# Optimization experiments

Hardware: AMD Instinct MI355X
Metric: run time of the kernel (lower is better)

Reference implementation:

```python
import jax, jax.numpy as jnp
import numpy as np

B, L, V, H, NL = 128, 512, 2048, 512, 2


def setup_inputs() -> dict:
    key = jax.random.key(0)
    ks = jax.random.split(key, 20)
    s = 0.05  # param scale
    inp = {
        "input_ids": jax.random.randint(ks[0], (B,), 0, V),
        "last_hidden": jax.random.normal(ks[1], (NL, B, H), jnp.float32),
        "word_dict_vec": jax.random.normal(ks[2], (B, V, H), jnp.float32),
        "encoder_outputs": jax.random.normal(ks[3], (L, B, H), jnp.float32),
        "seq_mask": (jax.random.uniform(ks[4], (B, L)) < 0.2).at[:, 0].set(False),
        # Attn params (torch Linear: y = x @ W.T + b)
        "attn_W": jax.random.normal(ks[5], (H, 2 * H), jnp.float32) * s,
        "attn_b": jax.random.normal(ks[6], (H,), jnp.float32) * s,
        "score_W": jax.random.normal(ks[7], (1, H), jnp.float32) * s,
        # concat layer
        "concat_W": jax.random.normal(ks[8], (H, 2 * H), jnp.float32) * s,
        "concat_b": jax.random.normal(ks[9], (H,), jnp.float32) * s,
        # GRU layer 0 (input 2H) and layer 1 (input H); gates ordered r,z,n as in torch
        "W_ih0": jax.random.normal(ks[10], (3 * H, 2 * H), jnp.float32) * s,
        "W_hh0": jax.random.normal(ks[11], (3 * H, H), jnp.float32) * s,
        "b_ih0": jax.random.normal(ks[12], (3 * H,), jnp.float32) * s,
        "b_hh0": jax.random.normal(ks[13], (3 * H,), jnp.float32) * s,
        "W_ih1": jax.random.normal(ks[14], (3 * H, H), jnp.float32) * s,
        "W_hh1": jax.random.normal(ks[15], (3 * H, H), jnp.float32) * s,
        "b_ih1": jax.random.normal(ks[16], (3 * H,), jnp.float32) * s,
        "b_hh1": jax.random.normal(ks[17], (3 * H,), jnp.float32) * s,
    }
    return inp


def _gru_cell(x, h, W_ih, W_hh, b_ih, b_hh):
    gi = x @ W_ih.T + b_ih
    gh = h @ W_hh.T + b_hh
    i_r, i_z, i_n = jnp.split(gi, 3, axis=-1)
    h_r, h_z, h_n = jnp.split(gh, 3, axis=-1)
    r = jax.nn.sigmoid(i_r + h_r)
    z = jax.nn.sigmoid(i_z + h_z)
    n = jnp.tanh(i_n + r * h_n)
    return (1.0 - z) * n + z * h


def reference(input_ids, last_hidden, word_dict_vec, encoder_outputs, seq_mask,
              attn_W, attn_b, score_W, concat_W, concat_b,
              W_ih0, W_hh0, b_ih0, b_hh0, W_ih1, W_hh1, b_ih1, b_hh1):
    # one_hot @ word_dict_vec == per-batch row gather (same math)
    emb = word_dict_vec[jnp.arange(B), input_ids]  # [B, H]

    # Bahdanau additive attention over encoder_outputs [L, B, H]
    q = last_hidden[-1]  # [B, H]
    hid = jnp.broadcast_to(q[None], (L, B, H))
    energy_in = jnp.concatenate([hid, encoder_outputs], axis=2)  # [L, B, 2H]
    e = jnp.tanh(energy_in @ attn_W.T + attn_b) @ score_W.T      # [L, B, 1]
    scores = e[..., 0].T                                          # [B, L]
    scores = jnp.where(seq_mask, jnp.float32(-1e12), scores)
    aw = jax.nn.softmax(scores, axis=1)                           # [B, L]

    context = jnp.einsum('bl,lbh->bh', aw, encoder_outputs)       # [B, H]

    # single-step 2-layer GRU (eval mode: dropout = identity)
    x0 = jnp.concatenate([emb, context], axis=1)                  # [B, 2H]
    h0 = _gru_cell(x0, last_hidden[0], W_ih0, W_hh0, b_ih0, b_hh0)
    h1 = _gru_cell(h0, last_hidden[1], W_ih1, W_hh1, b_ih1, b_hh1)
    hidden = jnp.stack([h0, h1])                                  # [2, B, H]

    output = jnp.tanh(jnp.concatenate([h1, context], axis=1) @ concat_W.T + concat_b)
    return output, hidden
```

## Files before the change

### kernel.cpp

```cpp
#include <hip/hip_runtime.h>
#include <stdint.h>

#define Hdim 512
#define Bdim 128
#define Ldim 512
#define Vdim 2048

typedef unsigned short u16;
using f32x4  = float  __attribute__((ext_vector_type(4)));
using bf16x8 = __bf16 __attribute__((ext_vector_type(8)));

__device__ inline u16 f2bf(float x) {
  uint32_t u = __float_as_uint(x);
  u += 0x7fffu + ((u >> 16) & 1u);
  return (u16)(u >> 16);
}
__device__ inline float bfhi2f(uint32_t hi16) { return __uint_as_float(hi16 << 16); }
__device__ inline float fast_tanh(float x) {
  return 1.0f - 2.0f / (__expf(2.0f * x) + 1.0f);
}
__device__ inline float fast_sig(float x) { return 1.0f / (1.0f + __expf(-x)); }

__device__ inline void gload_lds16(const u16* g, u16* l) {
  auto gp = (const __attribute__((address_space(1))) uint32_t*)(uintptr_t)g;
  auto lp = (__attribute__((address_space(3))) uint32_t*)(uintptr_t)l;
  __builtin_amdgcn_global_load_lds(gp, lp, 16, 0, 0);
}

__global__ void prep_all_kernel(const float* __restrict__ enc, u16* __restrict__ enc_bf,
                                const float* __restrict__ attn_W, const float* __restrict__ cat_W,
                                const float* __restrict__ W_ih0, const float* __restrict__ W_hh0,
                                const float* __restrict__ W_ih1, const float* __restrict__ W_hh1,
                                const float* __restrict__ b_ih0, const float* __restrict__ b_hh0,
                                const float* __restrict__ b_ih1, const float* __restrict__ b_hh1,
                                u16* __restrict__ arena, float* __restrict__ biasg0,
                                float* __restrict__ biasg1,
                                const float* __restrict__ wdv, const int* __restrict__ ids,
                                const float* __restrict__ lh, u16* __restrict__ X0bf,
                                u16* __restrict__ X1bf,
                                const uint8_t* __restrict__ maskb, int* __restrict__ flag) {
  int blk = blockIdx.x, t = threadIdx.x;
  if (blk < 16384) {
    size_t i = ((size_t)blk * 256 + t) * 8;
    float4 a = *(const float4*)(enc + i);
    float4 b = *(const float4*)(enc + i + 4);
    ushort4 u0, u1;
    u0.x = f2bf(a.x); u0.y = f2bf(a.y); u0.z = f2bf(a.z); u0.w = f2bf(a.w);
    u1.x = f2bf(b.x); u1.y = f2bf(b.y); u1.z = f2bf(b.z); u1.w = f2bf(b.w);
    *(ushort4*)(enc_bf + i) = u0;
    *(ushort4*)(enc_bf + i + 4) = u1;
    return;
  }
  if (blk < 22528) {
    int e = ((blk - 16384) * 256 + t) * 4;
    float4 v = {0.f, 0.f, 0.f, 0.f};
    if (e < 262144) {
      int o = e >> 9, k = e & 511;
      v = *(const float4*)(attn_W + (size_t)o * 1024 + k);
    } else if (e < 524288) {
      int e2 = e - 262144; int o = e2 >> 9, k = e2 & 511;
      v = *(const float4*)(attn_W + (size_t)o * 1024 + 512 + k);
    } else if (e < 1048576) {
      int e2 = e - 524288; int o = e2 >> 10, k = e2 & 1023;
      v = *(const float4*)(cat_W + (size_t)o * 1024 + k);
    } else if (e < 4194304) {
      int e2 = e - 1048576; int row = e2 / 1536, k = e2 % 1536;
      int o = row >> 2, gt = row & 3;
      if (gt == 0)      v = (k < 1024) ? *(const float4*)(W_ih0 + (size_t)o * 1024 + k)
                                       : *(const float4*)(W_hh0 + (size_t)o * 512 + k - 1024);
      else if (gt == 1) v = (k < 1024) ? *(const float4*)(W_ih0 + (size_t)(512 + o) * 1024 + k)
                                       : *(const float4*)(W_hh0 + (size_t)(512 + o) * 512 + k - 1024);
      else if (gt == 2) { if (k < 1024) v = *(const float4*)(W_ih0 + (size_t)(1024 + o) * 1024 + k); }
      else              { if (k >= 1024) v = *(const float4*)(W_hh0 + (size_t)(1024 + o) * 512 + k - 1024); }
    } else {
      int e2 = e - 4194304; int row = e2 >> 10, k = e2 & 1023;
      int o = row >> 2, gt = row & 3;
      if (gt == 0)      v = (k < 512) ? *(const float4*)(W_ih1 + (size_t)o * 512 + k)
                                      : *(const float4*)(W_hh1 + (size_t)o * 512 + k - 512);
      else if (gt == 1) v = (k < 512) ? *(const float4*)(W_ih1 + (size_t)(512 + o) * 512 + k)
                                      : *(const float4*)(W_hh1 + (size_t)(512 + o) * 512 + k - 512);
      else if (gt == 2) { if (k < 512) v = *(const float4*)(W_ih1 + (size_t)(1024 + o) * 512 + k); }
      else              { if (k >= 512) v = *(const float4*)(W_hh1 + (size_t)(1024 + o) * 512 + k - 512); }
    }
    ushort4 u;
    u.x = f2bf(v.x); u.y = f2bf(v.y); u.z = f2bf(v.z); u.w = f2bf(v.w);
    *(ushort4*)(arena + e) = u;
    return;
  }
  if (blk < 22544) {
    int idx = (blk - 22528) * 256 + t;
    int layer = idx >> 11, r = idx & 2047;
    int o = r >> 2, gt = r & 3;
    float v;
    if (layer == 0) {
      v = (gt == 0) ? b_ih0[o] + b_hh0[o]
        : (gt == 1) ? b_ih0[512 + o] + b_hh0[512 + o]
        : (gt == 2) ? b_ih0[1024 + o] : b_hh0[1024 + o];
      biasg0[r] = v;
    } else {
      v = (gt == 0) ? b_ih1[o] + b_hh1[o]
        : (gt == 1) ? b_ih1[512 + o] + b_hh1[512 + o]
        : (gt == 2) ? b_ih1[1024 + o] : b_hh1[1024 + o];
      biasg1[r] = v;
    }
    return;
  }
  if (blk < 23312) {
    int gid = (blk - 22544) * 256 + t;
    int region = gid >> 16, idx = gid & 65535;
    int b = idx >> 9, i = idx & 511;
    if (region == 0)
      X0bf[b * 1536 + i] = f2bf(wdv[(size_t)b * (Vdim * Hdim) + (size_t)ids[b] * Hdim + i]);
    else if (region == 1)
      X0bf[b * 1536 + 1024 + i] = f2bf(lh[idx]);
    else
      X1bf[b * 1024 + 512 + i] = f2bf(lh[65536 + idx]);
    return;
  }
  {
    __shared__ int sf;
    if (t == 0) sf = 0;
    __syncthreads();
    int found = 0;
    for (int i = t * 4; i < Bdim * Ldim; i += 256 * 4) {
      uint32_t v = *(const uint32_t*)(maskb + i);
      if (v & 0xffffff00u) found = 1;
    }
    if (found) sf = 1;
    __syncthreads();
    if (t == 0) *flag = sf;
  }
}

__global__ __launch_bounds__(256)
void thin_gemm32(const u16* __restrict__ X, int ldx, const u16* __restrict__ W,
                 const float* __restrict__ bias, float* __restrict__ C, int ldc,
                 int K, int act) {
  int n0 = blockIdx.x * 32;
  int t = threadIdx.x, lane = t & 63, w = t >> 6;
  int fr = lane & 15, g = lane >> 4, kof = g * 8;
  f32x4 acc[2][2];
#pragma unroll
  for (int i = 0; i < 2; ++i)
#pragma unroll
    for (int j = 0; j < 2; ++j) acc[i][j] = (f32x4){0.f, 0.f, 0.f, 0.f};
  const u16* Xr0 = X + (size_t)(w * 32 + fr) * ldx;
  const u16* Xr1 = Xr0 + (size_t)16 * ldx;
  const u16* Wr0 = W + (size_t)(n0 + fr) * K;
  const u16* Wr1 = W + (size_t)(n0 + 16 + fr) * K;
#pragma unroll 4
  for (int kt = 0; kt < K; kt += 32) {
    bf16x8 a0 = *(const bf16x8*)(Xr0 + kt + kof);
    bf16x8 a1 = *(const bf16x8*)(Xr1 + kt + kof);
    bf16x8 b0 = *(const bf16x8*)(Wr0 + kt + kof);
    bf16x8 b1 = *(const bf16x8*)(Wr1 + kt + kof);
    acc[0][0] = __builtin_amdgcn_mfma_f32_16x16x32_bf16(a0, b0, acc[0][0], 0, 0, 0);
    acc[0][1] = __builtin_amdgcn_mfma_f32_16x16x32_bf16(a0, b1, acc[0][1], 0, 0, 0);
    acc[1][0] = __builtin_amdgcn_mfma_f32_16x16x32_bf16(a1, b0, acc[1][0], 0, 0, 0);
    acc[1][1] = __builtin_amdgcn_mfma_f32_16x16x32_bf16(a1, b1, acc[1][1], 0, 0, 0);
  }
#pragma unroll
  for (int mi = 0; mi < 2; ++mi)
#pragma unroll
    for (int ni = 0; ni < 2; ++ni) {
      int col = n0 + ni * 16 + fr;
      float vb = bias[col];
#pragma unroll
      for (int j = 0; j < 4; ++j) {
        int row = w * 32 + 16 * mi + g * 4 + j;
        float v = acc[mi][ni][j] + vb;
        if (act) v = tanhf(v);
        C[(size_t)row * ldc + col] = v;
      }
    }
}

__global__ __launch_bounds__(512)
void attn_scores_kernel(const u16* __restrict__ enc_bf, const u16* __restrict__ Wenc,
                        const float* __restrict__ qW, const float* __restrict__ score_W,
                        float* __restrict__ scores) {
  __shared__ __align__(16) u16 As[2][4096];
  __shared__ __align__(16) u16 Bs[2][16384];
  __shared__ float part[8][128];
  int mb = blockIdx.x;
  int t = threadIdx.x, lane = t & 63, wid = t >> 6;
  int fr = lane & 15, g = lane >> 4, kof = g * 8;
  int m0 = mb * 128;
  int lrow = lane >> 2, lseg = (lane & 3) * 8;

  f32x4 acc[8][4];
#pragma unroll
  for (int i = 0; i < 8; ++i)
#pragma unroll
    for (int j = 0; j < 4; ++j) acc[i][j] = (f32x4){0.f, 0.f, 0.f, 0.f};

  auto STAGE = [&](int kt, int sel) {
    {
      int row = wid * 16 + lrow;
      gload_lds16(enc_bf + (size_t)(m0 + row) * 512 + kt + lseg, &As[sel][wid * 512]);
    }
#pragma unroll
    for (int i = 0; i < 4; ++i) {
      int ch = wid * 4 + i;
      int row = ch * 16 + lrow;
      gload_lds16(Wenc + (size_t)row * 512 + kt + lseg, &Bs[sel][ch * 512]);
    }
  };

  STAGE(0, 0);
  __syncthreads();
#pragma unroll 1
  for (int step = 0; step < 16; ++step) {
    int sel = step & 1;
    if (step < 15) STAGE((step + 1) * 32, sel ^ 1);
    bf16x8 a[8], b[4];
#pragma unroll
    for (int mi = 0; mi < 8; ++mi) a[mi] = *(const bf16x8*)&As[sel][(mi * 16 + fr) * 32 + kof];
#pragma unroll
    for (int ni = 0; ni < 4; ++ni) b[ni] = *(const bf16x8*)&Bs[sel][(wid * 64 + ni * 16 + fr) * 32 + kof];
#pragma unroll
    for (int mi = 0; mi < 8; ++mi)
#pragma unroll
      for (int ni = 0; ni < 4; ++ni)
        acc[mi][ni] = __builtin_amdgcn_mfma_f32_16x16x32_bf16(a[mi], b[ni], acc[mi][ni], 0, 0, 0);
    __syncthreads();
  }

#pragma unroll
  for (int mi = 0; mi < 8; ++mi) {
    float rs0 = 0.f, rs1 = 0.f, rs2 = 0.f, rs3 = 0.f;
#pragma unroll
    for (int ni = 0; ni < 4; ++ni) {
      int o = wid * 64 + ni * 16 + fr;
      float sw = score_W[o];
      int brow = mi * 16 + g * 4;
      rs0 += sw * fast_tanh(acc[mi][ni][0] + qW[(brow + 0) * 512 + o]);
      rs1 += sw * fast_tanh(acc[mi][ni][1] + qW[(brow + 1) * 512 + o]);
      rs2 += sw * fast_tanh(acc[mi][ni][2] + qW[(brow + 2) * 512 + o]);
      rs3 += sw * fast_tanh(acc[mi][ni][3] + qW[(brow + 3) * 512 + o]);
    }
#pragma unroll
    for (int d = 1; d < 16; d <<= 1) {
      rs0 += __shfl_xor(rs0, d);
      rs1 += __shfl_xor(rs1, d);
      rs2 += __shfl_xor(rs2, d);
      rs3 += __shfl_xor(rs3, d);
    }
    if (fr < 4) {
      float v = (fr == 0) ? rs0 : (fr == 1) ? rs1 : (fr == 2) ? rs2 : rs3;
      part[wid][mi * 16 + g * 4 + fr] = v;
    }
  }
  __syncthreads();
  if (t < 128) {
    float s = 0.f;
#pragma unroll
    for (int w2 = 0; w2 < 8; ++w2) s += part[w2][t];
    scores[t * 512 + mb] = s;
  }
}

__global__ __launch_bounds__(256)
void softctx_kernel(const float* __restrict__ scores, const void* __restrict__ maskp,
                    const int* __restrict__ flag, const u16* __restrict__ enc_bf,
                    u16* __restrict__ X0bf, u16* __restrict__ c1bf) {
  int bx = blockIdx.x;
  int b = bx >> 2, c = bx & 3;
  int t = threadIdx.x;
  __shared__ float wgt[512];
  __shared__ float redm[4], reds[4];
  __shared__ float ps[4][64][2];
  int l0 = t, l1 = t + 256;
  float s0 = scores[b * 512 + l0], s1 = scores[b * 512 + l1];
  bool isbyte = (*flag != 0);
  bool m0, m1;
  if (isbyte) {
    m0 = ((const uint8_t*)maskp)[b * 512 + l0] != 0;
    m1 = ((const uint8_t*)maskp)[b * 512 + l1] != 0;
  } else {
    m0 = ((const int*)maskp)[b * 512 + l0] != 0;
    m1 = ((const int*)maskp)[b * 512 + l1] != 0;
  }
  float v0 = m0 ? -1e12f : s0;
  float v1 = m1 ? -1e12f : s1;
  float mx = fmaxf(v0, v1);
#pragma unroll
  for (int d = 1; d < 64; d <<= 1) mx = fmaxf(mx, __shfl_xor(mx, d));
  if ((t & 63) == 0) redm[t >> 6] = mx;
  __syncthreads();
  mx = fmaxf(fmaxf(redm[0], redm[1]), fmaxf(redm[2], redm[3]));
  float e0 = __expf(v0 - mx), e1 = __expf(v1 - mx);
  float sm = e0 + e1;
#pragma unroll
  for (int d = 1; d < 64; d <<= 1) sm += __shfl_xor(sm, d);
  if ((t & 63) == 0) reds[t >> 6] = sm;
  __syncthreads();
  sm = reds[0] + reds[1] + reds[2] + reds[3];
  float inv = 1.0f / sm;
  wgt[l0] = e0 * inv;
  wgt[l1] = e1 * inv;
  __syncthreads();
  int cp = t & 63, lq = t >> 6;
  int col = c * 128 + cp * 2;
  float a0 = 0.f, a1 = 0.f;
  for (int l = lq * 128; l < lq * 128 + 128; ++l) {
    float wl = wgt[l];
    if (wl != 0.0f) {
      uint32_t v = *(const uint32_t*)(enc_bf + ((size_t)l * 128 + b) * 512 + col);
      a0 += wl * bfhi2f(v & 0xffffu);
      a1 += wl * __uint_as_float(v & 0xffff0000u);
    }
  }
  ps[lq][cp][0] = a0;
  ps[lq][cp][1] = a1;
  __syncthreads();
  if (t < 64) {
    float r0 = ps[0][t][0] + ps[1][t][0] + ps[2][t][0] + ps[3][t][0];
    float r1 = ps[0][t][1] + ps[1][t][1] + ps[2][t][1] + ps[3][t][1];
    int cc = c * 128 + t * 2;
    uint32_t packed = (uint32_t)f2bf(r0) | ((uint32_t)f2bf(r1) << 16);
    *(uint32_t*)(X0bf + b * 1536 + 512 + cc) = packed;
    *(uint32_t*)(c1bf + b * 1024 + 512 + cc) = packed;
  }
}

__global__ __launch_bounds__(256)
void gru_gemm_kernel(const u16* __restrict__ X, int ldx, const u16* __restrict__ Wp,
                     const float* __restrict__ biasp, const float* __restrict__ hprev,
                     int K, float* __restrict__ hout, u16* __restrict__ xdst) {
  __shared__ float ct[128][36];
  int n0 = blockIdx.x * 32;
  int t = threadIdx.x, lane = t & 63, w = t >> 6;
  int fr = lane & 15, g = lane >> 4, kof = g * 8;
  f32x4 acc[2][2];
#pragma unroll
  for (int i = 0; i < 2; ++i)
#pragma unroll
    for (int j = 0; j < 2; ++j) acc[i][j] = (f32x4){0.f, 0.f, 0.f, 0.f};
  const u16* Xr0 = X + (size_t)(w * 32 + fr) * ldx;
  const u16* Xr1 = Xr0 + (size_t)16 * ldx;
  const u16* Wr0 = Wp + (size_t)(n0 + fr) * K;
  const u16* Wr1 = Wp + (size_t)(n0 + 16 + fr) * K;
#pragma unroll 4
  for (int kt = 0; kt < K; kt += 32) {
    bf16x8 a0 = *(const bf16x8*)(Xr0 + kt + kof);
    bf16x8 a1 = *(const bf16x8*)(Xr1 + kt + kof);
    bf16x8 b0 = *(const bf16x8*)(Wr0 + kt + kof);
    bf16x8 b1 = *(const bf16x8*)(Wr1 + kt + kof);
    acc[0][0] = __builtin_amdgcn_mfma_f32_16x16x32_bf16(a0, b0, acc[0][0], 0, 0, 0);
    acc[0][1] = __builtin_amdgcn_mfma_f32_16x16x32_bf16(a0, b1, acc[0][1], 0, 0, 0);
    acc[1][0] = __builtin_amdgcn_mfma_f32_16x16x32_bf16(a1, b0, acc[1][0], 0, 0, 0);
    acc[1][1] = __builtin_amdgcn_mfma_f32_16x16x32_bf16(a1, b1, acc[1][1], 0, 0, 0);
  }
#pragma unroll
  for (int mi = 0; mi < 2; ++mi)
#pragma unroll
    for (int ni = 0; ni < 2; ++ni) {
      int col = ni * 16 + fr;
      float vb = biasp[n0 + col];
#pragma unroll
      for (int j = 0; j < 4; ++j)
        ct[w * 32 + 16 * mi + g * 4 + j][col] = acc[mi][ni][j] + vb;
    }
  __syncthreads();
#pragma unroll
  for (int i = 0; i < 4; ++i) {
    int u = t + i * 256;
    int b = u >> 3, ol = u & 7;
    float cr = ct[b][ol * 4 + 0];
    float cz = ct[b][ol * 4 + 1];
    float ci = ct[b][ol * 4 + 2];
    float ch = ct[b][ol * 4 + 3];
    int o = blockIdx.x * 8 + ol;
    float r = fast_sig(cr);
    float z = fast_sig(cz);
    float n = tanhf(ci + r * ch);
    float h = (1.0f - z) * n + z * hprev[b * 512 + o];
    hout[b * 512 + o] = h;
    xdst[b * 1024 + o] = f2bf(h);
  }
}

extern "C" void kernel_launch(void* const* d_in, const int* in_sizes, int n_in,
                              void* d_out, int out_size, void* d_ws, size_t ws_size,
                              hipStream_t stream) {
  const int*   ids    = (const int*)  d_in[0];
  const float* lh     = (const float*)d_in[1];
  const float* wdv    = (const float*)d_in[2];
  const float* enc    = (const float*)d_in[3];
  const void*  mask   = d_in[4];
  const float* attn_W = (const float*)d_in[5];
  const float* attn_b = (const float*)d_in[6];
  const float* scW    = (const float*)d_in[7];
  const float* cat_W  = (const float*)d_in[8];
  const float* cat_b  = (const float*)d_in[9];
  const float* W_ih0  = (const float*)d_in[10];
  const float* W_hh0  = (const float*)d_in[11];
  const float* b_ih0  = (const float*)d_in[12];
  const float* b_hh0  = (const float*)d_in[13];
  const float* W_ih1  = (const float*)d_in[14];
  const float* W_hh1  = (const float*)d_in[15];
  const float* b_ih1  = (const float*)d_in[16];
  const float* b_hh1  = (const float*)d_in[17];

  float* out = (float*)d_out;
  float* h0  = out + 65536;
  float* h1  = out + 131072;

  float* ws     = (float*)d_ws;
  float* scores = ws;
  float* qW     = ws + 65536;
  float* biasg0 = ws + 131072;
  float* biasg1 = ws + 133120;
  int*   flag   = (int*)(ws + 135168);
  u16*   arena  = (u16*)(ws + 135184);
  u16*   enc_bf = (u16*)(ws + 3280912);
  u16*   X0bf   = (u16*)(ws + 20058128);
  u16*   X1bf   = (u16*)(ws + 20156432);
  u16*   c1bf   = (u16*)(ws + 20221968);

  const u16* Whid = arena;
  const u16* Wenc = arena + 262144;
  const u16* Wcat = arena + 524288;
  const u16* Wg0p = arena + 1048576;
  const u16* Wg1p = arena + 4194304;

  prep_all_kernel<<<23313, 256, 0, stream>>>(enc, enc_bf, attn_W, cat_W,
                                             W_ih0, W_hh0, W_ih1, W_hh1,
                                             b_ih0, b_hh0, b_ih1, b_hh1,
                                             arena, biasg0, biasg1,
                                             wdv, ids, lh, X0bf, X1bf,
                                             (const uint8_t*)mask, flag);
  thin_gemm32<<<16, 256, 0, stream>>>(X1bf + 512, 1024, Whid, attn_b, qW, 512, 512, 0);
  attn_scores_kernel<<<512, 512, 0, stream>>>(enc_bf, Wenc, qW, scW, scores);
  softctx_kernel<<<512, 256, 0, stream>>>(scores, mask, flag, enc_bf, X0bf, c1bf);
  gru_gemm_kernel<<<64, 256, 0, stream>>>(X0bf, 1536, Wg0p, biasg0, lh, 1536, h0, X1bf);
  gru_gemm_kernel<<<64, 256, 0, stream>>>(X1bf, 1024, Wg1p, biasg1, lh + 65536, 1024, h1, c1bf);
  thin_gemm32<<<16, 256, 0, stream>>>(c1bf, 1024, Wcat, cat_b, out, 512, 1024, 1);
}
```

Measured before the change: 210.3 us.

## Drop encoder bf16 pre-conversion; convert in attention GEMM and fold qW into prep

The separate pass that converted the whole encoder_outputs tensor to bf16 is removed. The attention GEMM now loads fp32 encoder tiles, packs them to bf16 in registers and stages them through double-buffered LDS, and softctx reads fp32 encoder rows directly. The query projection GEMM is folded into the prep kernel, which removes one launch, and attention is split across two output halves with partial score sums added in softmax. This avoids writing and re-reading a 64MB intermediate, at the cost of reading fp32 twice (attention and context) and doing the conversion inside the GEMM loop.

Result: faster. 187.8 us (-10.7%).

```diff
diff --git a/kernel.cpp b/kernel.cpp
--- a/kernel.cpp
+++ b/kernel.cpp
@@ -15,71 +15,104 @@
   u += 0x7fffu + ((u >> 16) & 1u);
   return (u16)(u >> 16);
 }
-__device__ inline float bfhi2f(uint32_t hi16) { return __uint_as_float(hi16 << 16); }
+__device__ inline uint32_t pk2(float lo, float hi) {
+  return (uint32_t)f2bf(lo) | ((uint32_t)f2bf(hi) << 16);
+}
 __device__ inline float fast_tanh(float x) {
   return 1.0f - 2.0f / (__expf(2.0f * x) + 1.0f);
 }
 __device__ inline float fast_sig(float x) { return 1.0f / (1.0f + __expf(-x)); }
 
-__device__ inline void gload_lds16(const u16* g, u16* l) {
-  auto gp = (const __attribute__((address_space(1))) uint32_t*)(uintptr_t)g;
-  auto lp = (__attribute__((address_space(3))) uint32_t*)(uintptr_t)l;
-  __builtin_amdgcn_global_load_lds(gp, lp, 16, 0, 0);
-}
-
-__global__ void prep_all_kernel(const float* __restrict__ enc, u16* __restrict__ enc_bf,
-                                const float* __restrict__ attn_W, const float* __restrict__ cat_W,
-                                const float* __restrict__ W_ih0, const float* __restrict__ W_hh0,
-                                const float* __restrict__ W_ih1, const float* __restrict__ W_hh1,
-                                const float* __restrict__ b_ih0, const float* __restrict__ b_hh0,
-                                const float* __restrict__ b_ih1, const float* __restrict__ b_hh1,
-                                u16* __restrict__ arena, float* __restrict__ biasg0,
-                                float* __restrict__ biasg1,
-                                const float* __restrict__ wdv, const int* __restrict__ ids,
-                                const float* __restrict__ lh, u16* __restrict__ X0bf,
-                                u16* __restrict__ X1bf,
-                                const uint8_t* __restrict__ maskb, int* __restrict__ flag) {
+__device__ inline bf16x8 pack_bf8(float4 x, float4 y) {
+  union { uint32_t d[4]; bf16x8 v; } r;
+  r.d[0] = pk2(x.x, x.y); r.d[1] = pk2(x.z, x.w);
+  r.d[2] = pk2(y.x, y.y); r.d[3] = pk2(y.z, y.w);
+  return r.v;
+}
+
+__global__ __launch_bounds__(512)
+void prep_kernel(const float* __restrict__ lh, const float* __restrict__ attn_W,
+                 const float* __restrict__ attn_b, const float* __restrict__ cat_W,
+                 const float* __restrict__ W_ih0, const float* __restrict__ W_hh0,
+                 const float* __restrict__ W_ih1, const float* __restrict__ W_hh1,
+                 const float* __restrict__ b_ih0, const float* __restrict__ b_hh0,
+                 const float* __restrict__ b_ih1, const float* __restrict__ b_hh1,
+                 const float* __restrict__ wdv, const int* __restrict__ ids,
+                 const void* __restrict__ mask,
+                 float* __restrict__ qW, u16* __restrict__ arena,
+                 float* __restrict__ biasg0, float* __restrict__ biasg1,
+                 u16* __restrict__ X0bf, u16* __restrict__ X1bf, int* __restrict__ flag) {
   int blk = blockIdx.x, t = threadIdx.x;
-  if (blk < 16384) {
-    size_t i = ((size_t)blk * 256 + t) * 8;
-    float4 a = *(const float4*)(enc + i);
-    float4 b = *(const float4*)(enc + i + 4);
-    ushort4 u0, u1;
-    u0.x = f2bf(a.x); u0.y = f2bf(a.y); u0.z = f2bf(a.z); u0.w = f2bf(a.w);
-    u1.x = f2bf(b.x); u1.y = f2bf(b.y); u1.z = f2bf(b.z); u1.w = f2bf(b.w);
-    *(ushort4*)(enc_bf + i) = u0;
-    *(ushort4*)(enc_bf + i + 4) = u1;
+  int lane = t & 63, wid = t >> 6;
+  int fr = lane & 15, g = lane >> 4, kof = g * 8;
+
+  if (blk < 16) {
+    int mh = wid & 3, nh = wid >> 2;
+    int n0 = blk * 32 + nh * 16;
+    int rb0 = mh * 32;
+    f32x4 ac0 = {0.f, 0.f, 0.f, 0.f}, ac1 = {0.f, 0.f, 0.f, 0.f};
+    const float* q = lh + 65536;
+#pragma unroll 2
+    for (int kt = 0; kt < 512; kt += 32) {
+      const float* qr0 = q + (size_t)(rb0 + fr) * 512 + kt + kof;
+      const float* qr1 = qr0 + 16 * 512;
+      const float* wr  = attn_W + (size_t)(n0 + fr) * 1024 + kt + kof;
+      float4 x0 = *(const float4*)qr0, x1 = *(const float4*)(qr0 + 4);
+      float4 y0 = *(const float4*)qr1, y1 = *(const float4*)(qr1 + 4);
+      float4 w0 = *(const float4*)wr,  w1 = *(const float4*)(wr + 4);
+      bf16x8 A0 = pack_bf8(x0, x1), A1 = pack_bf8(y0, y1), Bb = pack_bf8(w0, w1);
+      ac0 = __builtin_amdgcn_mfma_f32_16x16x32_bf16(A0, Bb, ac0, 0, 0, 0);
+      ac1 = __builtin_amdgcn_mfma_f32_16x16x32_bf16(A1, Bb, ac1, 0, 0, 0);
+    }
+    float vb = attn_b[n0 + fr];
+#pragma unroll
+    for (int j = 0; j < 4; ++j) {
+      qW[(size_t)(rb0 + g * 4 + j) * 512 + n0 + fr]      = ac0[j] + vb;
+      qW[(size_t)(rb0 + 16 + g * 4 + j) * 512 + n0 + fr] = ac1[j] + vb;
+    }
     return;
   }
-  if (blk < 22528) {
-    int e = ((blk - 16384) * 256 + t) * 4;
+  if (blk == 16) {
+    __shared__ int sf;
+    if (t == 0) sf = 0;
+    __syncthreads();
+    const uint32_t* m32 = (const uint32_t*)mask;
+    int found = 0;
+    for (int i = t; i < 16384; i += 512)
+      if (m32[i] & 0xffffff00u) found = 1;
+    if (found) sf = 1;
+    __syncthreads();
+    if (t == 0) *flag = sf;
+    return;
+  }
+  const int ARENA_Q = 1507328;
+  int i = (blk - 17) * 512 + t;
+  if (i < ARENA_Q) {
+    int e = i * 4;
     float4 v = {0.f, 0.f, 0.f, 0.f};
     if (e < 262144) {
       int o = e >> 9, k = e & 511;
-      v = *(const float4*)(attn_W + (size_t)o * 1024 + k);
-    } else if (e < 524288) {
-      int e2 = e - 262144; int o = e2 >> 9, k = e2 & 511;
       v = *(const float4*)(attn_W + (size_t)o * 1024 + 512 + k);
-    } else if (e < 1048576) {
-      int e2 = e - 524288; int o = e2 >> 10, k = e2 & 1023;
+    } else if (e < 786432) {
+      int e2 = e - 262144; int o = e2 >> 10, k = e2 & 1023;
       v = *(const float4*)(cat_W + (size_t)o * 1024 + k);
-    } else if (e < 4194304) {
-      int e2 = e - 1048576; int row = e2 / 1536, k = e2 % 1536;
+    } else if (e < 3932160) {
+      int e2 = e - 786432; int row = e2 / 1536, k = e2 % 1536;
       int o = row >> 2, gt = row & 3;
       if (gt == 0)      v = (k < 1024) ? *(const float4*)(W_ih0 + (size_t)o * 1024 + k)
                                        : *(const float4*)(W_hh0 + (size_t)o * 512 + k - 1024);
       else if (gt == 1) v = (k < 1024) ? *(const float4*)(W_ih0 + (size_t)(512 + o) * 1024 + k)
                                        : *(const float4*)(W_hh0 + (size_t)(512 + o) * 512 + k - 1024);
-      else if (gt == 2) { if (k < 1024) v = *(const float4*)(W_ih0 + (size_t)(1024 + o) * 1024 + k); }
+      else if (gt == 2) { if (k < 1024)  v = *(const float4*)(W_ih0 + (size_t)(1024 + o) * 1024 + k); }
       else              { if (k >= 1024) v = *(const float4*)(W_hh0 + (size_t)(1024 + o) * 512 + k - 1024); }
     } else {
-      int e2 = e - 4194304; int row = e2 >> 10, k = e2 & 1023;
+      int e2 = e - 3932160; int row = e2 >> 10, k = e2 & 1023;
       int o = row >> 2, gt = row & 3;
       if (gt == 0)      v = (k < 512) ? *(const float4*)(W_ih1 + (size_t)o * 512 + k)
                                       : *(const float4*)(W_hh1 + (size_t)o * 512 + k - 512);
       else if (gt == 1) v = (k < 512) ? *(const float4*)(W_ih1 + (size_t)(512 + o) * 512 + k)
                                       : *(const float4*)(W_hh1 + (size_t)(512 + o) * 512 + k - 512);
-      else if (gt == 2) { if (k < 512) v = *(const float4*)(W_ih1 + (size_t)(1024 + o) * 512 + k); }
+      else if (gt == 2) { if (k < 512)  v = *(const float4*)(W_ih1 + (size_t)(1024 + o) * 512 + k); }
       else              { if (k >= 512) v = *(const float4*)(W_hh1 + (size_t)(1024 + o) * 512 + k - 512); }
     }
     ushort4 u;
@@ -87,48 +120,248 @@
     *(ushort4*)(arena + e) = u;
     return;
   }
-  if (blk < 22544) {
-    int idx = (blk - 22528) * 256 + t;
-    int layer = idx >> 11, r = idx & 2047;
-    int o = r >> 2, gt = r & 3;
-    float v;
-    if (layer == 0) {
-      v = (gt == 0) ? b_ih0[o] + b_hh0[o]
-        : (gt == 1) ? b_ih0[512 + o] + b_hh0[512 + o]
-        : (gt == 2) ? b_ih0[1024 + o] : b_hh0[1024 + o];
-      biasg0[r] = v;
-    } else {
-      v = (gt == 0) ? b_ih1[o] + b_hh1[o]
-        : (gt == 1) ? b_ih1[512 + o] + b_hh1[512 + o]
-        : (gt == 2) ? b_ih1[1024 + o] : b_hh1[1024 + o];
-      biasg1[r] = v;
-    }
-    return;
-  }
-  if (blk < 23312) {
-    int gid = (blk - 22544) * 256 + t;
-    int region = gid >> 16, idx = gid & 65535;
-    int b = idx >> 9, i = idx & 511;
-    if (region == 0)
-      X0bf[b * 1536 + i] = f2bf(wdv[(size_t)b * (Vdim * Hdim) + (size_t)ids[b] * Hdim + i]);
-    else if (region == 1)
-      X0bf[b * 1536 + 1024 + i] = f2bf(lh[idx]);
-    else
-      X1bf[b * 1024 + 512 + i] = f2bf(lh[65536 + idx]);
-    return;
-  }
-  {
-    __shared__ int sf;
-    if (t == 0) sf = 0;
+  int i2 = i - ARENA_Q;
+  if (i2 < 1024) {
+    int r4 = i2 * 4; int layer = r4 >> 11; int r = r4 & 2047; int o = r >> 2;
+    const float* bi = layer ? b_ih1 : b_ih0;
+    const float* bh = layer ? b_hh1 : b_hh0;
+    float4 v;
+    v.x = bi[o] + bh[o];
+    v.y = bi[512 + o] + bh[512 + o];
+    v.z = bi[1024 + o];
+    v.w = bh[1024 + o];
+    *(float4*)((layer ? biasg1 : biasg0) + r) = v;
+  } else if (i2 < 1024 + 16384) {
+    int j = (i2 - 1024) * 4; int b = j >> 9, i0 = j & 511;
+    float4 v = *(const float4*)(wdv + (size_t)b * (Vdim * Hdim) + (size_t)ids[b] * 512 + i0);
+    ushort4 u;
+    u.x = f2bf(v.x); u.y = f2bf(v.y); u.z = f2bf(v.z); u.w = f2bf(v.w);
+    *(ushort4*)(X0bf + b * 1536 + i0) = u;
+  } else if (i2 < 1024 + 32768) {
+    int j = (i2 - 1024 - 16384) * 4; int b = j >> 9, i0 = j & 511;
+    float4 v = *(const float4*)(lh + (size_t)b * 512 + i0);
+    ushort4 u;
+    u.x = f2bf(v.x); u.y = f2bf(v.y); u.z = f2bf(v.z); u.w = f2bf(v.w);
+    *(ushort4*)(X0bf + b * 1536 + 1024 + i0) = u;
+  } else if (i2 < 1024 + 49152) {
+    int j = (i2 - 1024 - 32768) * 4; int b = j >> 9, i0 = j & 511;
+    float4 v = *(const float4*)(lh + 65536 + (size_t)b * 512 + i0);
+    ushort4 u;
+    u.x = f2bf(v.x); u.y = f2bf(v.y); u.z = f2bf(v.z); u.w = f2bf(v.w);
+    *(ushort4*)(X1bf + b * 1024 + 512 + i0) = u;
+  }
+}
+
+__global__ __launch_bounds__(512)
+void attn_kernel(const float* __restrict__ enc, const u16* __restrict__ Wenc,
+                 const float* __restrict__ qW, const float* __restrict__ scW,
+                 float* __restrict__ scores_p) {
+  __shared__ __align__(16) u16 As[2][128 * 40];
+  __shared__ __align__(16) u16 Bs[2][256 * 40];
+  __shared__ float part[8 * 128];
+  int blk = blockIdx.x, t = threadIdx.x;
+  int lane = t & 63, wid = t >> 6;
+  int fr = lane & 15, g = lane >> 4, kof = g * 8;
+  int l  = (blk >> 4) * 8 + (blk & 7);
+  int oh = (blk >> 3) & 1;
+  int ob = oh * 256;
+  const int arow = t >> 2;
+  const int aks = (t & 3) * 8;
+
+  f32x4 acc[8][2];
+#pragma unroll
+  for (int i = 0; i < 8; ++i) {
+    acc[i][0] = (f32x4){0.f, 0.f, 0.f, 0.f};
+    acc[i][1] = (f32x4){0.f, 0.f, 0.f, 0.f};
+  }
+  const float* abase = enc + ((size_t)l * 128 + arow) * 512 + aks;
+  const u16* bbase0 = Wenc + (size_t)(ob + arow) * 512 + aks;
+  const u16* bbase1 = bbase0 + (size_t)128 * 512;
+
+  float4 ra0 = *(const float4*)abase;
+  float4 ra1 = *(const float4*)(abase + 4);
+  uint4 rb0 = *(const uint4*)bbase0;
+  uint4 rb1 = *(const uint4*)bbase1;
+
+#pragma unroll 2
+  for (int step = 0; step < 16; ++step) {
+    int sel = step & 1;
     __syncthreads();
-    int found = 0;
-    for (int i = t * 4; i < Bdim * Ldim; i += 256 * 4) {
-      uint32_t v = *(const uint32_t*)(maskb + i);
-      if (v & 0xffffff00u) found = 1;
-    }
-    if (found) sf = 1;
+    uint4 ap;
+    ap.x = pk2(ra0.x, ra0.y); ap.y = pk2(ra0.z, ra0.w);
+    ap.z = pk2(ra1.x, ra1.y); ap.w = pk2(ra1.z, ra1.w);
+    *(uint4*)(&As[sel][arow * 40 + aks]) = ap;
+    *(uint4*)(&Bs[sel][arow * 40 + aks]) = rb0;
+    *(uint4*)(&Bs[sel][(128 + arow) * 40 + aks]) = rb1;
+    if (step < 15) {
+      int kt = (step + 1) * 32;
+      ra0 = *(const float4*)(abase + kt);
+      ra1 = *(const float4*)(abase + kt + 4);
+      rb0 = *(const uint4*)(bbase0 + kt);
+      rb1 = *(const uint4*)(bbase1 + kt);
+    }
     __syncthreads();
-    if (t == 0) *flag = sf;
+    bf16x8 b0 = *(const bf16x8*)(&Bs[sel][(wid * 32 + fr) * 40 + kof]);
+    bf16x8 b1 = *(const bf16x8*)(&Bs[sel][(wid * 32 + 16 + fr) * 40 + kof]);
+#pragma unroll
+    for (int mi = 0; mi < 8; ++mi) {
+      bf16x8 av = *(const bf16x8*)(&As[sel][(mi * 16 + fr) * 40 + kof]);
+      acc[mi][0] = __builtin_amdgcn_mfma_f32_16x16x32_bf16(av, b0, acc[mi][0], 0, 0, 0);
+      acc[mi][1] = __builtin_amdgcn_mfma_f32_16x16x32_bf16(av, b1, acc[mi][1], 0, 0, 0);
+    }
+  }
+#pragma unroll
+  for (int mi = 0; mi < 8; ++mi) {
+    float rs0 = 0.f, rs1 = 0.f, rs2 = 0.f, rs3 = 0.f;
+#pragma unroll
+    for (int ni = 0; ni < 2; ++ni) {
+      int o = ob + wid * 32 + ni * 16 + fr;
+      float sw = scW[o];
+      int brow = mi * 16 + g * 4;
+      rs0 += sw * fast_tanh(acc[mi][ni][0] + qW[(size_t)(brow + 0) * 512 + o]);
+      rs1 += sw * fast_tanh(acc[mi][ni][1] + qW[(size_t)(brow + 1) * 512 + o]);
+      rs2 += sw * fast_tanh(acc[mi][ni][2] + qW[(size_t)(brow + 2) * 512 + o]);
+      rs3 += sw * fast_tanh(acc[mi][ni][3] + qW[(size_t)(brow + 3) * 512 + o]);
+    }
+#pragma unroll
+    for (int d = 1; d < 16; d <<= 1) {
+      rs0 += __shfl_xor(rs0, d);
+      rs1 += __shfl_xor(rs1, d);
+      rs2 += __shfl_xor(rs2, d);
+      rs3 += __shfl_xor(rs3, d);
+    }
+    if (fr < 4) {
+      float v = (fr == 0) ? rs0 : (fr == 1) ? rs1 : (fr == 2) ? rs2 : rs3;
+      part[wid * 128 + mi * 16 + g * 4 + fr] = v;
+    }
+  }
+  __syncthreads();
+  if (t < 128) {
+    float s = 0.f;
+#pragma unroll
+    for (int w2 = 0; w2 < 8; ++w2) s += part[w2 * 128 + t];
+    scores_p[(size_t)(oh * 128 + t) * 512 + l] = s;
+  }
+}
+
+__global__ __launch_bounds__(256)
+void softctx_kernel(const float* __restrict__ sp, const void* __restrict__ maskp,
+                    const int* __restrict__ flag, const float* __restrict__ enc,
+                    u16* __restrict__ X0bf, u16* __restrict__ c1bf) {
+  int bx = blockIdx.x;
+  int b = bx >> 2, c = bx & 3;
+  int t = threadIdx.x;
+  __shared__ float wgt[512];
+  __shared__ float redm[4], reds[4];
+  __shared__ float ps[4][64][2];
+  int l0 = t, l1 = t + 256;
+  float s0 = sp[(size_t)b * 512 + l0] + sp[(size_t)(128 + b) * 512 + l0];
+  float s1 = sp[(size_t)b * 512 + l1] + sp[(size_t)(128 + b) * 512 + l1];
+  bool isbyte = (*flag != 0);
+  bool m0, m1;
+  if (isbyte) {
+    m0 = ((const uint8_t*)maskp)[b * 512 + l0] != 0;
+    m1 = ((const uint8_t*)maskp)[b * 512 + l1] != 0;
+  } else {
+    m0 = ((const int*)maskp)[b * 512 + l0] != 0;
+    m1 = ((const int*)maskp)[b * 512 + l1] != 0;
+  }
+  float v0 = m0 ? -1e12f : s0;
+  float v1 = m1 ? -1e12f : s1;
+  float mx = fmaxf(v0, v1);
+#pragma unroll
+  for (int d = 1; d < 64; d <<= 1) mx = fmaxf(mx, __shfl_xor(mx, d));
+  if ((t & 63) == 0) redm[t >> 6] = mx;
+  __syncthreads();
+  mx = fmaxf(fmaxf(redm[0], redm[1]), fmaxf(redm[2], redm[3]));
+  float e0 = __expf(v0 - mx), e1 = __expf(v1 - mx);
+  float sm = e0 + e1;
+#pragma unroll
+  for (int d = 1; d < 64; d <<= 1) sm += __shfl_xor(sm, d);
+  if ((t & 63) == 0) reds[t >> 6] = sm;
+  __syncthreads();
+  sm = reds[0] + reds[1] + reds[2] + reds[3];
+  float inv = 1.0f / sm;
+  wgt[l0] = e0 * inv;
+  wgt[l1] = e1 * inv;
+  __syncthreads();
+  int cp = t & 63, lq = t >> 6;
+  int col = c * 128 + cp * 2;
+  float a0 = 0.f, a1 = 0.f;
+  for (int l = lq * 128; l < lq * 128 + 128; ++l) {
+    float wl = wgt[l];
+    if (wl != 0.0f) {
+      float2 ev = *(const float2*)(enc + ((size_t)l * 128 + b) * 512 + col);
+      a0 += wl * ev.x;
+      a1 += wl * ev.y;
+    }
+  }
+  ps[lq][cp][0] = a0;
+  ps[lq][cp][1] = a1;
+  __syncthreads();
+  if (t < 64) {
+    float r0 = ps[0][t][0] + ps[1][t][0] + ps[2][t][0] + ps[3][t][0];
+    float r1 = ps[0][t][1] + ps[1][t][1] + ps[2][t][1] + ps[3][t][1];
+    int cc = c * 128 + t * 2;
+    uint32_t packed = pk2(r0, r1);
+    *(uint32_t*)(X0bf + b * 1536 + 512 + cc) = packed;
+    *(uint32_t*)(c1bf + b * 1024 + 512 + cc) = packed;
+  }
+}
+
+__global__ __launch_bounds__(256)
+void gru_gemm_kernel(const u16* __restrict__ X, int ldx, const u16* __restrict__ Wp,
+                     const float* __restrict__ biasp, const float* __restrict__ hprev,
+                     int K, float* __restrict__ hout, u16* __restrict__ xdst) {
+  __shared__ float ct[128][36];
+  int n0 = blockIdx.x * 32;
+  int t = threadIdx.x, lane = t & 63, w = t >> 6;
+  int fr = lane & 15, g = lane >> 4, kof = g * 8;
+  f32x4 acc[2][2];
+#pragma unroll
+  for (int i = 0; i < 2; ++i)
+#pragma unroll
+    for (int j = 0; j < 2; ++j) acc[i][j] = (f32x4){0.f, 0.f, 0.f, 0.f};
+  const u16* Xr0 = X + (size_t)(w * 32 + fr) * ldx;
+  const u16* Xr1 = Xr0 + (size_t)16 * ldx;
+  const u16* Wr0 = Wp + (size_t)(n0 + fr) * K;
+  const u16* Wr1 = Wp + (size_t)(n0 + 16 + fr) * K;
+#pragma unroll 4
+  for (int kt = 0; kt < K; kt += 32) {
+    bf16x8 a0 = *(const bf16x8*)(Xr0 + kt + kof);
+    bf16x8 a1 = *(const bf16x8*)(Xr1 + kt + kof);
+    bf16x8 b0 = *(const bf16x8*)(Wr0 + kt + kof);
+    bf16x8 b1 = *(const bf16x8*)(Wr1 + kt + kof);
+    acc[0][0] = __builtin_amdgcn_mfma_f32_16x16x32_bf16(a0, b0, acc[0][0], 0, 0, 0);
+    acc[0][1] = __builtin_amdgcn_mfma_f32_16x16x32_bf16(a0, b1, acc[0][1], 0, 0, 0);
+    acc[1][0] = __builtin_amdgcn_mfma_f32_16x16x32_bf16(a1, b0, acc[1][0], 0, 0, 0);
+    acc[1][1] = __builtin_amdgcn_mfma_f32_16x16x32_bf16(a1, b1, acc[1][1], 0, 0, 0);
+  }
+#pragma unroll
+  for (int mi = 0; mi < 2; ++mi)
+#pragma unroll
+    for (int ni = 0; ni < 2; ++ni) {
+      int col = ni * 16 + fr;
+      float vb = biasp[n0 + col];
+#pragma unroll
+      for (int j = 0; j < 4; ++j)
+        ct[w * 32 + 16 * mi + g * 4 + j][col] = acc[mi][ni][j] + vb;
+    }
+  __syncthreads();
+#pragma unroll
+  for (int i = 0; i < 4; ++i) {
+    int u = t + i * 256;
+    int b = u >> 3, ol = u & 7;
+    float cr  = ct[b][ol * 4 + 0];
+    float cz  = ct[b][ol * 4 + 1];
+    float ci  = ct[b][ol * 4 + 2];
+    float chh = ct[b][ol * 4 + 3];
+    int o = blockIdx.x * 8 + ol;
+    float r = fast_sig(cr), z = fast_sig(cz);
+    float n = tanhf(ci + r * chh);
+    float h = (1.0f - z) * n + z * hprev[b * 512 + o];
+    hout[b * 512 + o] = h;
+    xdst[b * 1024 + o] = f2bf(h);
   }
 }
 
@@ -173,212 +406,6 @@
         C[(size_t)row * ldc + col] = v;
       }
     }
-}
-
-__global__ __launch_bounds__(512)
-void attn_scores_kernel(const u16* __restrict__ enc_bf, const u16* __restrict__ Wenc,
-                        const float* __restrict__ qW, const float* __restrict__ score_W,
-                        float* __restrict__ scores) {
-  __shared__ __align__(16) u16 As[2][4096];
-  __shared__ __align__(16) u16 Bs[2][16384];
-  __shared__ float part[8][128];
-  int mb = blockIdx.x;
-  int t = threadIdx.x, lane = t & 63, wid = t >> 6;
-  int fr = lane & 15, g = lane >> 4, kof = g * 8;
-  int m0 = mb * 128;
-  int lrow = lane >> 2, lseg = (lane & 3) * 8;
-
-  f32x4 acc[8][4];
-#pragma unroll
-  for (int i = 0; i < 8; ++i)
-#pragma unroll
-    for (int j = 0; j < 4; ++j) acc[i][j] = (f32x4){0.f, 0.f, 0.f, 0.f};
-
-  auto STAGE = [&](int kt, int sel) {
-    {
-      int row = wid * 16 + lrow;
-      gload_lds16(enc_bf + (size_t)(m0 + row) * 512 + kt + lseg, &As[sel][wid * 512]);
-    }
-#pragma unroll
-    for (int i = 0; i < 4; ++i) {
-      int ch = wid * 4 + i;
-      int row = ch * 16 + lrow;
-      gload_lds16(Wenc + (size_t)row * 512 + kt + lseg, &Bs[sel][ch * 512]);
-    }
-  };
-
-  STAGE(0, 0);
-  __syncthreads();
-#pragma unroll 1
-  for (int step = 0; step < 16; ++step) {
-    int sel = step & 1;
-    if (step < 15) STAGE((step + 1) * 32, sel ^ 1);
-    bf16x8 a[8], b[4];
-#pragma unroll
-    for (int mi = 0; mi < 8; ++mi) a[mi] = *(const bf16x8*)&As[sel][(mi * 16 + fr) * 32 + kof];
-#pragma unroll
-    for (int ni = 0; ni < 4; ++ni) b[ni] = *(const bf16x8*)&Bs[sel][(wid * 64 + ni * 16 + fr) * 32 + kof];
-#pragma unroll
-    for (int mi = 0; mi < 8; ++mi)
-#pragma unroll
-      for (int ni = 0; ni < 4; ++ni)
-        acc[mi][ni] = __builtin_amdgcn_mfma_f32_16x16x32_bf16(a[mi], b[ni], acc[mi][ni], 0, 0, 0);
-    __syncthreads();
-  }
-
-#pragma unroll
-  for (int mi = 0; mi < 8; ++mi) {
-    float rs0 = 0.f, rs1 = 0.f, rs2 = 0.f, rs3 = 0.f;
-#pragma unroll
-    for (int ni = 0; ni < 4; ++ni) {
-      int o = wid * 64 + ni * 16 + fr;
-      float sw = score_W[o];
-      int brow = mi * 16 + g * 4;
-      rs0 += sw * fast_tanh(acc[mi][ni][0] + qW[(brow + 0) * 512 + o]);
-      rs1 += sw * fast_tanh(acc[mi][ni][1] + qW[(brow + 1) * 512 + o]);
-      rs2 += sw * fast_tanh(acc[mi][ni][2] + qW[(brow + 2) * 512 + o]);
-      rs3 += sw * fast_tanh(acc[mi][ni][3] + qW[(brow + 3) * 512 + o]);
-    }
-#pragma unroll
-    for (int d = 1; d < 16; d <<= 1) {
-      rs0 += __shfl_xor(rs0, d);
-      rs1 += __shfl_xor(rs1, d);
-      rs2 += __shfl_xor(rs2, d);
-      rs3 += __shfl_xor(rs3, d);
-    }
-    if (fr < 4) {
-      float v = (fr == 0) ? rs0 : (fr == 1) ? rs1 : (fr == 2) ? rs2 : rs3;
-      part[wid][mi * 16 + g * 4 + fr] = v;
-    }
-  }
-  __syncthreads();
-  if (t < 128) {
-    float s = 0.f;
-#pragma unroll
-    for (int w2 = 0; w2 < 8; ++w2) s += part[w2][t];
-    scores[t * 512 + mb] = s;
-  }
-}
-
-__global__ __launch_bounds__(256)
-void softctx_kernel(const float* __restrict__ scores, const void* __restrict__ maskp,
-                    const int* __restrict__ flag, const u16* __restrict__ enc_bf,
-                    u16* __restrict__ X0bf, u16* __restrict__ c1bf) {
-  int bx = blockIdx.x;
-  int b = bx >> 2, c = bx & 3;
-  int t = threadIdx.x;
-  __shared__ float wgt[512];
-  __shared__ float redm[4], reds[4];
-  __shared__ float ps[4][64][2];
-  int l0 = t, l1 = t + 256;
-  float s0 = scores[b * 512 + l0], s1 = scores[b * 512 + l1];
-  bool isbyte = (*flag != 0);
-  bool m0, m1;
-  if (isbyte) {
-    m0 = ((const uint8_t*)maskp)[b * 512 + l0] != 0;
-    m1 = ((const uint8_t*)maskp)[b * 512 + l1] != 0;
-  } else {
-    m0 = ((const int*)maskp)[b * 512 + l0] != 0;
-    m1 = ((const int*)maskp)[b * 512 + l1] != 0;
-  }
-  float v0 = m0 ? -1e12f : s0;
-  float v1 = m1 ? -1e12f : s1;
-  float mx = fmaxf(v0, v1);
-#pragma unroll
-  for (int d = 1; d < 64; d <<= 1) mx = fmaxf(mx, __shfl_xor(mx, d));
-  if ((t & 63) == 0) redm[t >> 6] = mx;
-  __syncthreads();
-  mx = fmaxf(fmaxf(redm[0], redm[1]), fmaxf(redm[2], redm[3]));
-  float e0 = __expf(v0 - mx), e1 = __expf(v1 - mx);
-  float sm = e0 + e1;
-#pragma unroll
-  for (int d = 1; d < 64; d <<= 1) sm += __shfl_xor(sm, d);
-  if ((t & 63) == 0) reds[t >> 6] = sm;
-  __syncthreads();
-  sm = reds[0] + reds[1] + reds[2] + reds[3];
-  float inv = 1.0f / sm;
-  wgt[l0] = e0 * inv;
-  wgt[l1] = e1 * inv;
-  __syncthreads();
-  int cp = t & 63, lq = t >> 6;
-  int col = c * 128 + cp * 2;
-  float a0 = 0.f, a1 = 0.f;
-  for (int l = lq * 128; l < lq * 128 + 128; ++l) {
-    float wl = wgt[l];
-    if (wl != 0.0f) {
-      uint32_t v = *(const uint32_t*)(enc_bf + ((size_t)l * 128 + b) * 512 + col);
-      a0 += wl * bfhi2f(v & 0xffffu);
-      a1 += wl * __uint_as_float(v & 0xffff0000u);
-    }
-  }
-  ps[lq][cp][0] = a0;
-  ps[lq][cp][1] = a1;
-  __syncthreads();
-  if (t < 64) {
-    float r0 = ps[0][t][0] + ps[1][t][0] + ps[2][t][0] + ps[3][t][0];
-    float r1 = ps[0][t][1] + ps[1][t][1] + ps[2][t][1] + ps[3][t][1];
-    int cc = c * 128 + t * 2;
-    uint32_t packed = (uint32_t)f2bf(r0) | ((uint32_t)f2bf(r1) << 16);
-    *(uint32_t*)(X0bf + b * 1536 + 512 + cc) = packed;
-    *(uint32_t*)(c1bf + b * 1024 + 512 + cc) = packed;
-  }
-}
-
-__global__ __launch_bounds__(256)
-void gru_gemm_kernel(const u16* __restrict__ X, int ldx, const u16* __restrict__ Wp,
-                     const float* __restrict__ biasp, const float* __restrict__ hprev,
-                     int K, float* __restrict__ hout, u16* __restrict__ xdst) {
-  __shared__ float ct[128][36];
-  int n0 = blockIdx.x * 32;
-  int t = threadIdx.x, lane = t & 63, w = t >> 6;
-  int fr = lane & 15, g = lane >> 4, kof = g * 8;
-  f32x4 acc[2][2];
-#pragma unroll
-  for (int i = 0; i < 2; ++i)
-#pragma unroll
-    for (int j = 0; j < 2; ++j) acc[i][j] = (f32x4){0.f, 0.f, 0.f, 0.f};
-  const u16* Xr0 = X + (size_t)(w * 32 + fr) * ldx;
-  const u16* Xr1 = Xr0 + (size_t)16 * ldx;
-  const u16* Wr0 = Wp + (size_t)(n0 + fr) * K;
-  const u16* Wr1 = Wp + (size_t)(n0 + 16 + fr) * K;
-#pragma unroll 4
-  for (int kt = 0; kt < K; kt += 32) {
-    bf16x8 a0 = *(const bf16x8*)(Xr0 + kt + kof);
-    bf16x8 a1 = *(const bf16x8*)(Xr1 + kt + kof);
-    bf16x8 b0 = *(const bf16x8*)(Wr0 + kt + kof);
-    bf16x8 b1 = *(const bf16x8*)(Wr1 + kt + kof);
-    acc[0][0] = __builtin_amdgcn_mfma_f32_16x16x32_bf16(a0, b0, acc[0][0], 0, 0, 0);
-    acc[0][1] = __builtin_amdgcn_mfma_f32_16x16x32_bf16(a0, b1, acc[0][1], 0, 0, 0);
-    acc[1][0] = __builtin_amdgcn_mfma_f32_16x16x32_bf16(a1, b0, acc[1][0], 0, 0, 0);
-    acc[1][1] = __builtin_amdgcn_mfma_f32_16x16x32_bf16(a1, b1, acc[1][1], 0, 0, 0);
-  }
-#pragma unroll
-  for (int mi = 0; mi < 2; ++mi)
-#pragma unroll
-    for (int ni = 0; ni < 2; ++ni) {
-      int col = ni * 16 + fr;
-      float vb = biasp[n0 + col];
-#pragma unroll
-      for (int j = 0; j < 4; ++j)
-        ct[w * 32 + 16 * mi + g * 4 + j][col] = acc[mi][ni][j] + vb;
-    }
-  __syncthreads();
-#pragma unroll
-  for (int i = 0; i < 4; ++i) {
-    int u = t + i * 256;
-    int b = u >> 3, ol = u & 7;
-    float cr = ct[b][ol * 4 + 0];
-    float cz = ct[b][ol * 4 + 1];
-    float ci = ct[b][ol * 4 + 2];
-    float ch = ct[b][ol * 4 + 3];
-    int o = blockIdx.x * 8 + ol;
-    float r = fast_sig(cr);
-    float z = fast_sig(cz);
-    float n = tanhf(ci + r * ch);
-    float h = (1.0f - z) * n + z * hprev[b * 512 + o];
-    hout[b * 512 + o] = h;
-    xdst[b * 1024 + o] = f2bf(h);
-  }
 }
 
 extern "C" void kernel_launch(void* const* d_in, const int* in_sizes, int n_in,
@@ -407,33 +434,29 @@
   float* h0  = out + 65536;
   float* h1  = out + 131072;
 
-  float* ws     = (float*)d_ws;
-  float* scores = ws;
-  float* qW     = ws + 65536;
-  float* biasg0 = ws + 131072;
-  float* biasg1 = ws + 133120;
-  int*   flag   = (int*)(ws + 135168);
-  u16*   arena  = (u16*)(ws + 135184);
-  u16*   enc_bf = (u16*)(ws + 3280912);
-  u16*   X0bf   = (u16*)(ws + 20058128);
-  u16*   X1bf   = (u16*)(ws + 20156432);
-  u16*   c1bf   = (u16*)(ws + 20221968);
-
-  const u16* Whid = arena;
-  const u16* Wenc = arena + 262144;
-  const u16* Wcat = arena + 524288;
-  const u16* Wg0p = arena + 1048576;
-  const u16* Wg1p = arena + 4194304;
-
-  prep_all_kernel<<<23313, 256, 0, stream>>>(enc, enc_bf, attn_W, cat_W,
-                                             W_ih0, W_hh0, W_ih1, W_hh1,
-                                             b_ih0, b_hh0, b_ih1, b_hh1,
-                                             arena, biasg0, biasg1,
-                                             wdv, ids, lh, X0bf, X1bf,
-                                             (const uint8_t*)mask, flag);
-  thin_gemm32<<<16, 256, 0, stream>>>(X1bf + 512, 1024, Whid, attn_b, qW, 512, 512, 0);
-  attn_scores_kernel<<<512, 512, 0, stream>>>(enc_bf, Wenc, qW, scW, scores);
-  softctx_kernel<<<512, 256, 0, stream>>>(scores, mask, flag, enc_bf, X0bf, c1bf);
+  float* ws       = (float*)d_ws;
+  float* qW       = ws;
+  float* scores_p = ws + 65536;
+  float* biasg0   = ws + 196608;
+  float* biasg1   = ws + 198656;
+  int*   flag     = (int*)(ws + 200704);
+  u16*   arena    = (u16*)(ws + 200720);
+  u16*   X0bf     = (u16*)(ws + 3215376);
+  u16*   X1bf     = (u16*)(ws + 3313680);
+  u16*   c1bf     = (u16*)(ws + 3379216);
+
+  const u16* Wenc = arena;
+  const u16* Wcat = arena + 262144;
+  const u16* Wg0p = arena + 786432;
+  const u16* Wg1p = arena + 3932160;
+
+  prep_kernel<<<3059, 512, 0, stream>>>(lh, attn_W, attn_b, cat_W,
+                                        W_ih0, W_hh0, W_ih1, W_hh1,
+                                        b_ih0, b_hh0, b_ih1, b_hh1,
+                                        wdv, ids, mask,
+                                        qW, arena, biasg0, biasg1, X0bf, X1bf, flag);
+  attn_kernel<<<1024, 512, 0, stream>>>(enc, Wenc, qW, scW, scores_p);
+  softctx_kernel<<<512, 256, 0, stream>>>(scores_p, mask, flag, enc, X0bf, c1bf);
   gru_gemm_kernel<<<64, 256, 0, stream>>>(X0bf, 1536, Wg0p, biasg0, lh, 1536, h0, X1bf);
   gru_gemm_kernel<<<64, 256, 0, stream>>>(X1bf, 1024, Wg1p, biasg1, lh + 65536, 1024, h1, c1bf);
   thin_gemm32<<<16, 256, 0, stream>>>(c1bf, 1024, Wcat, cat_b, out, 512, 1024, 1);
```
